# Kernel tuning notes

Measured on AMD Instinct MI355X. Metric: run time of the kernel, lower is better.

The kernel has to match this reference:

```python
import jax, jax.numpy as jnp
from jax import lax
import numpy as np

B, T, N = 64, 512, 80
HT, HV, HI = 512, 1024, 512  # textual, visual, ilstm hidden sizes


def setup_inputs() -> dict:
    key = jax.random.key(0)
    ks = jax.random.split(key, 12)
    s = 0.02
    return {
        "h_v": jax.random.normal(ks[0], (B, T, HV), jnp.float32),
        "h_s": jax.random.normal(ks[1], (B, N, HT), jnp.float32),
        "W_S": jax.random.normal(ks[2], (HI, HT), jnp.float32) * s,
        "b_S": jnp.zeros((HI,), jnp.float32),
        "W_V": jax.random.normal(ks[3], (HI, HV), jnp.float32) * s,
        "b_V": jnp.zeros((HI,), jnp.float32),
        "W_R": jax.random.normal(ks[4], (HI, HI), jnp.float32) * s,
        "b_R": jnp.zeros((HI,), jnp.float32),
        "W_w": jax.random.normal(ks[5], (1, HI), jnp.float32) * s,
        "b_w": jnp.zeros((1,), jnp.float32),
        "W_ih": jax.random.normal(ks[6], (4 * HI, HT + HV), jnp.float32) * s,
        "b_ih": jnp.zeros((4 * HI,), jnp.float32),
        "W_hh": jax.random.normal(ks[7], (4 * HI, HI), jnp.float32) * s,
        "b_hh": jnp.zeros((4 * HI,), jnp.float32),
    }


def reference(h_v, h_s, W_S, b_S, W_V, b_V, W_R, b_R, W_w, b_w, W_ih, b_ih, W_hh, b_hh):
    n_batch, T_, _ = h_v.shape
    Hi = W_R.shape[0]
    dt = h_v.dtype
    # loop-invariant textual projection, hoisted: (B, N, Hi)
    S_proj = jnp.einsum('bnt,it->bni', h_s, W_S) + b_S
    # visual projection for all timesteps: (B, T, Hi)
    V_proj = jnp.einsum('btv,iv->bti', h_v, W_V) + b_V

    def step(carry, xs):
        h_prev, c_prev = carry
        v_t, hv_t = xs  # (B, Hi), (B, Hv)
        r_proj = h_prev @ W_R.T + b_R  # (B, Hi)
        pre = jnp.tanh(S_proj + (r_proj + v_t)[:, None, :])  # (B, N, Hi)
        beta = jnp.einsum('bni,i->bn', pre, W_w[0]) + b_w[0]  # (B, N)
        # NOTE: faithful to source -- softmax over the BATCH dim (dim=0)
        alpha = jax.nn.softmax(beta, axis=0)
        H_t_s = jnp.einsum('bnt,bn->bt', h_s, alpha)  # (B, Ht)
        r_t = jnp.concatenate([hv_t, H_t_s], axis=1)  # (B, Hv+Ht)
        gates = r_t @ W_ih.T + b_ih + h_prev @ W_hh.T + b_hh  # (B, 4Hi)
        i_g, f_g, g_g, o_g = jnp.split(gates, 4, axis=1)
        c_new = jax.nn.sigmoid(f_g) * c_prev + jax.nn.sigmoid(i_g) * jnp.tanh(g_g)
        h_new = jax.nn.sigmoid(o_g) * jnp.tanh(c_new)
        return (h_new, c_new), h_new

    init = (jnp.zeros((n_batch, Hi), dt), jnp.zeros((n_batch, Hi), dt))
    xs = (jnp.swapaxes(V_proj, 0, 1), jnp.swapaxes(h_v, 0, 1))  # time-major
    _, hs = lax.scan(step, init, xs)  # (T, B, Hi)
    return jnp.swapaxes(hs, 0, 1)  # (B, T, Hi)
```

## Files before the change

kernel.cpp:

```cpp
#include <hip/hip_runtime.h>


typedef unsigned short ushort_t;
typedef unsigned int uint_t;
typedef __attribute__((ext_vector_type(8))) short bf16x8;
typedef __attribute__((ext_vector_type(4))) float f32x4;

#define MFMA_BF16 __builtin_amdgcn_mfma_f32_16x16x32_bf16

__device__ __forceinline__ float bf2f(ushort_t u) {
  return __builtin_bit_cast(float, (uint_t)u << 16);
}
__device__ __forceinline__ ushort_t f2bf(float f) {
  uint_t u = __builtin_bit_cast(uint_t, f);
  u += 0x7FFFu + ((u >> 16) & 1u);
  return (ushort_t)(u >> 16);
}
__device__ __forceinline__ uint_t pk(float lo, float hi) {
  return (uint_t)f2bf(lo) | ((uint_t)f2bf(hi) << 16);
}
__device__ __forceinline__ void stage16(ushort_t* dst, const float* src) {
  float4 a = *(const float4*)src,     b = *(const float4*)(src + 4);
  float4 c = *(const float4*)(src + 8), d = *(const float4*)(src + 12);
  uint4 lo = { pk(a.x,a.y), pk(a.z,a.w), pk(b.x,b.y), pk(b.z,b.w) };
  uint4 hi = { pk(c.x,c.y), pk(c.z,c.w), pk(d.x,d.y), pk(d.z,d.w) };
  *(uint4*)dst = lo; *(uint4*)(dst + 8) = hi;
}
__device__ __forceinline__ bf16x8 cvt8(const float* src) {
  float4 a = *(const float4*)src, b = *(const float4*)(src + 4);
  uint4 u = { pk(a.x,a.y), pk(a.z,a.w), pk(b.x,b.y), pk(b.z,b.w) };
  return __builtin_bit_cast(bf16x8, u);
}
__device__ __forceinline__ float tanh_(float x) {
  float e = __expf(2.f * x);
  return 1.f - 2.f * __builtin_amdgcn_rcpf(e + 1.f);
}
__device__ __forceinline__ float sigm_(float x) {
  return __builtin_amdgcn_rcpf(1.f + __expf(-x));
}

__device__ __forceinline__ float ldcg_f(const float* p) {
  return __hip_atomic_load(p, __ATOMIC_RELAXED, __HIP_MEMORY_SCOPE_AGENT);
}
__device__ __forceinline__ void stcg_f(float* p, float v) {
  __hip_atomic_store(p, v, __ATOMIC_RELAXED, __HIP_MEMORY_SCOPE_AGENT);
}
__device__ __forceinline__ uint_t ldcg_u(const uint_t* p) {
  return __hip_atomic_load(p, __ATOMIC_RELAXED, __HIP_MEMORY_SCOPE_AGENT);
}
__device__ __forceinline__ void stcg_u(uint_t* p, uint_t v) {
  __hip_atomic_store(p, v, __ATOMIC_RELAXED, __HIP_MEMORY_SCOPE_AGENT);
}

__global__ __launch_bounds__(256) void cvt_kernel(
    const float* __restrict__ in, ushort_t* __restrict__ out, int n4) {
  int i = blockIdx.x * blockDim.x + threadIdx.x;
  if (i < n4) {
    float4 v = ((const float4*)in)[i];
    uint2 r = { pk(v.x, v.y), pk(v.z, v.w) };
    ((uint2*)out)[i] = r;
  }
}

__global__ __launch_bounds__(256) void pack_frag_kernel(
    const float* __restrict__ src, int ld, int coff,
    ushort_t* __restrict__ out, int mode, int lkc) {
  size_t o = ((size_t)blockIdx.x * 256 + threadIdx.x) * 8;
  int lane = (int)((o >> 3) & 63);
  int kc   = (int)((o >> 9) & ((1u << lkc) - 1u));
  int tile = (int)(o >> (9 + lkc));
  int row  = mode ? ((tile & 3) * 512 + (tile >> 2) * 16 + (lane & 15))
                  : (tile * 16 + (lane & 15));
  int col  = kc * 32 + (lane >> 4) * 8;
  const float* s = &src[(size_t)row * ld + coff + col];
  float4 a = *(const float4*)s, b = *(const float4*)(s + 4);
  uint4 u = { pk(a.x,a.y), pk(a.z,a.w), pk(b.x,b.y), pk(b.z,b.w) };
  *(uint4*)&out[o] = u;
}

__global__ __launch_bounds__(256) void gemm_bt(
    const float* __restrict__ A, int lda,
    const float* __restrict__ W, int ldw,
    const float* __restrict__ bias1,
    ushort_t* __restrict__ out, int ldo, int K, int tmaj)
{
  __shared__ __align__(16) ushort_t sA[128][32];
  __shared__ __align__(16) ushort_t sW[128][32];
  const int tid = threadIdx.x;
  const int col0 = blockIdx.x * 128, row0 = blockIdx.y * 128;
  const int lane = tid & 63, wv = tid >> 6;
  const int wr = (wv & 1) * 64, wc = (wv >> 1) * 64;
  const int fr = lane & 15, quad = lane >> 4;
  const int sr = tid >> 1, skk = (tid & 1) * 16;
  f32x4 acc[4][4] = {};
  for (int k0 = 0; k0 < K; k0 += 32) {
    stage16(&sA[sr][skk], &A[(size_t)(row0 + sr) * lda + k0 + skk]);
    stage16(&sW[sr][skk], &W[(size_t)(col0 + sr) * ldw + k0 + skk]);
    __syncthreads();
    bf16x8 af[4], wf[4];
    #pragma unroll
    for (int mt = 0; mt < 4; ++mt) af[mt] = *(const bf16x8*)&sA[wr + mt*16 + fr][quad*8];
    #pragma unroll
    for (int nt = 0; nt < 4; ++nt) wf[nt] = *(const bf16x8*)&sW[wc + nt*16 + fr][quad*8];
    #pragma unroll
    for (int mt = 0; mt < 4; ++mt)
      #pragma unroll
      for (int nt = 0; nt < 4; ++nt)
        acc[mt][nt] = MFMA_BF16(af[mt], wf[nt], acc[mt][nt], 0, 0, 0);
    __syncthreads();
  }
  #pragma unroll
  for (int nt = 0; nt < 4; ++nt) {
    int col = col0 + wc + nt*16 + fr;
    float bs = bias1 ? bias1[col] : 0.f;
    #pragma unroll
    for (int mt = 0; mt < 4; ++mt)
      #pragma unroll
      for (int r = 0; r < 4; ++r) {
        int row = row0 + wr + mt*16 + quad*4 + r;
        int orow = tmaj ? ((row & 511) * 64 + (row >> 9)) : row;
        out[(size_t)orow * ldo + col] = f2bf(acc[mt][nt][r] + bs);
      }
  }
}

__device__ __forceinline__ void spin_gen(unsigned* gen, unsigned g, unsigned* dead) {
  int n = 0;
  while (__hip_atomic_load(gen, __ATOMIC_RELAXED, __HIP_MEMORY_SCOPE_AGENT) == g) {
    __builtin_amdgcn_s_sleep(4);
    if (++n > 20000) {
      __hip_atomic_store(dead, 1u, __ATOMIC_RELAXED, __HIP_MEMORY_SCOPE_AGENT);
      break;
    }
    if ((n & 1023) == 0 &&
        __hip_atomic_load(dead, __ATOMIC_RELAXED, __HIP_MEMORY_SCOPE_AGENT) != 0u)
      break;
  }
}

__device__ __forceinline__ void sync_bar(unsigned* base, unsigned sub,
                                         unsigned sub_last, unsigned* dead) {
  __syncthreads();
  if (threadIdx.x == 0) {
    unsigned* gen = base + 288;
    if (__hip_atomic_load(dead, __ATOMIC_RELAXED, __HIP_MEMORY_SCOPE_AGENT) == 0u) {
      unsigned g = __hip_atomic_load(gen, __ATOMIC_RELAXED, __HIP_MEMORY_SCOPE_AGENT);
      unsigned old = __hip_atomic_fetch_add(base + sub * 32, 1u,
                        __ATOMIC_RELAXED, __HIP_MEMORY_SCOPE_AGENT);
      if (old == sub_last) {
        unsigned r = __hip_atomic_fetch_add(base + 256, 1u,
                        __ATOMIC_RELAXED, __HIP_MEMORY_SCOPE_AGENT);
        if (r == 7u) {
          #pragma unroll
          for (int i = 0; i < 8; ++i)
            __hip_atomic_store(base + i * 32, 0u, __ATOMIC_RELAXED, __HIP_MEMORY_SCOPE_AGENT);
          __hip_atomic_store(base + 256, 0u, __ATOMIC_RELAXED, __HIP_MEMORY_SCOPE_AGENT);
          __builtin_amdgcn_s_waitcnt(0);
          __hip_atomic_store(gen, g + 1u, __ATOMIC_RELAXED, __HIP_MEMORY_SCOPE_AGENT);
        } else {
          spin_gen(gen, g, dead);
        }
      } else {
        spin_gen(gen, g, dead);
      }
    }
  }
  __syncthreads();
}

struct LoopArgs {
  const ushort_t *Sproj, *Vproj, *Xproj;
  const ushort_t *WRf, *Whhf, *Wqf, *Wihf;
  const ushort_t *hsb;
  const float *bR, *Ww, *bih, *bhh, *hv;
  float *ru, *expb, *s4;
  uint_t *hrep, *hsrep;
  unsigned *bar;
  float *out;
};


__global__ __launch_bounds__(512, 2) void loop_kernel(LoopArgs p) {
  const int blk = blockIdx.x, tid = threadIdx.x;
  const int lane = tid & 63, wv = tid >> 6;
  const int fr = lane & 15, quad = lane >> 4;
  const int G = blk >> 6, w6 = blk & 63;
  const int b4 = G * 16 + (w6 & 15), q = w6 >> 4;
  const bool isGate = (w6 < 32);
  const bool isRu   = (w6 >= 32) && (w6 < 36);
  const int jt = w6 & 31;
  const int g = wv & 3, kh = wv >> 2;
  const int ct = ((w6 - 32) & 3) * 8 + wv;

  unsigned* dead = p.bar + 320;
  unsigned* rcnt = p.bar + 384 + G;
  unsigned* gbar = p.bar + 512 + G * 512;

  __shared__ __align__(16) uint_t sH[4096];
  __shared__ __align__(16) float s_ru[512];
  __shared__ __align__(16) float s_ww[512];
  __shared__ __align__(16) float s_red[512];
  __shared__ __align__(16) float s_acc[8][256];
  __shared__ float s_hsv[128];
  __shared__ float s_alpha[80];
  __shared__ float s_hh[256];
  __shared__ float s_bias[64];

  s_ww[tid] = p.Ww[tid];
  if (isGate && tid < 64) {
    int n = (tid >> 4) * 512 + jt * 16 + (tid & 15);
    s_bias[tid] = p.bih[n] + p.bhh[n];
  }
  float c_reg = 0.f;

  bf16x8 wf2[16];
  bf16x8 wfx[16];
  if (isGate) {
    #pragma unroll
    for (int kc = 0; kc < 8; ++kc) {
      int kcg = kh * 8 + kc;
      wf2[kc]     = *(const bf16x8*)&p.Whhf[((size_t)(jt*4+g)*16 + kcg)*512 + lane*8];
      wf2[8 + kc] = *(const bf16x8*)&p.Wqf [((size_t)(jt*4+g)*16 + kcg)*512 + lane*8];
    }
    if (!p.Xproj) {
      #pragma unroll
      for (int kc = 0; kc < 16; ++kc)
        wfx[kc] = *(const bf16x8*)&p.Wihf[((size_t)(jt*4+g)*32 + kh*16 + kc)*512 + lane*8];
    }
  } else if (isRu) {
    #pragma unroll
    for (int kc = 0; kc < 16; ++kc)
      wf2[kc] = *(const bf16x8*)&p.WRf[((size_t)ct*16 + kc)*512 + lane*8];
  }
  __syncthreads();

  f32x4 accA = {};
  for (int t = 0; t < 512; ++t) {
    float x0 = 0.f, x1 = 0.f, x2 = 0.f, x3 = 0.f;
    if (isGate) {
      f32x4 acc = {};
      if (!p.Xproj) {
        int row = G * 16 + fr;
        #pragma unroll
        for (int kc = 0; kc < 16; ++kc) {
          bf16x8 af = cvt8(&p.hv[((size_t)row * 512 + t) * 1024 + kh*512 + kc*32 + quad*8]);
          acc = MFMA_BF16(af, wfx[kc], acc, 0, 0, 0);
        }
      }
      if (t) {
        const uint_t* src = p.hrep + G * 4096;
        uint_t hst[8];
        #pragma unroll
        for (int i = 0; i < 8; ++i) hst[i] = ldcg_u(src + i * 512 + tid);
        #pragma unroll
        for (int i = 0; i < 8; ++i) sH[i * 512 + tid] = hst[i];
        __syncthreads();
        #pragma unroll
        for (int kc = 0; kc < 8; ++kc) {
          int kcg = kh * 8 + kc;
          bf16x8 af = *(const bf16x8*)&sH[kcg * 256 + quad * 64 + fr * 4];
          acc = MFMA_BF16(af, wf2[kc], acc, 0, 0, 0);
        }
      }
      accA = acc;
      if (p.Xproj && tid < 256) {
        const ushort_t* xp = &p.Xproj[(size_t)t * 131072 +
                                      (size_t)(G * 16 + (tid >> 4)) * 2048 + jt * 16 + (tid & 15)];
        x0 = bf2f(xp[0]);    x1 = bf2f(xp[512]);
        x2 = bf2f(xp[1024]); x3 = bf2f(xp[1536]);
      }
    } else if (isRu) {
      f32x4 acc = {};
      if (t) {
        const uint_t* src = p.hrep + G * 4096;
        uint_t hst[8];
        #pragma unroll
        for (int i = 0; i < 8; ++i) hst[i] = ldcg_u(src + i * 512 + tid);
        #pragma unroll
        for (int i = 0; i < 8; ++i) sH[i * 512 + tid] = hst[i];
        __syncthreads();
        #pragma unroll
        for (int kc = 0; kc < 16; ++kc) {
          bf16x8 af = *(const bf16x8*)&sH[kc * 256 + quad * 64 + fr * 4];
          acc = MFMA_BF16(af, wf2[kc], acc, 0, 0, 0);
        }
      }
      #pragma unroll
      for (int r = 0; r < 4; ++r) {
        int row = G * 16 + quad * 4 + r, col = ct * 16 + fr;
        float v = acc[r] + p.bR[col] + bf2f(p.Vproj[(size_t)t * 32768 + row * 512 + col]);
        stcg_f(&p.ru[row * 512 + col], v);
      }
      __syncthreads();
      if (tid == 0)
        __hip_atomic_fetch_add(rcnt, 1u, __ATOMIC_RELAXED, __HIP_MEMORY_SCOPE_AGENT);
    }

    if (tid == 0) {
      unsigned thr = 4u * (unsigned)(t + 1);
      int n = 0;
      while (ldcg_u(rcnt) < thr) {
        __builtin_amdgcn_s_sleep(4);
        if (++n > 20000) {
          stcg_u(dead, 1u);
          break;
        }
        if ((n & 1023) == 0 && ldcg_u(dead) != 0u) break;
      }
    }
    __syncthreads();
    s_ru[tid] = ldcg_f(&p.ru[b4 * 512 + tid]);
    __syncthreads();
    #pragma unroll
    for (int rr = 0; rr < 3; ++rr) {
      int nl = wv + 8 * rr;
      if (nl < 20) {
        int n = q * 20 + nl;
        uint4 sv = *(const uint4*)&p.Sproj[((size_t)(b4 * 80 + n)) * 512 + lane * 8];
        float4 r0 = *(const float4*)&s_ru[lane * 8];
        float4 r1 = *(const float4*)&s_ru[lane * 8 + 4];
        float4 w0 = *(const float4*)&s_ww[lane * 8];
        float4 w1 = *(const float4*)&s_ww[lane * 8 + 4];
        float a = 0.f;
        a += tanh_(bf2f((ushort_t)(sv.x & 0xFFFF)) + r0.x) * w0.x;
        a += tanh_(bf2f((ushort_t)(sv.x >> 16))    + r0.y) * w0.y;
        a += tanh_(bf2f((ushort_t)(sv.y & 0xFFFF)) + r0.z) * w0.z;
        a += tanh_(bf2f((ushort_t)(sv.y >> 16))    + r0.w) * w0.w;
        a += tanh_(bf2f((ushort_t)(sv.z & 0xFFFF)) + r1.x) * w1.x;
        a += tanh_(bf2f((ushort_t)(sv.z >> 16))    + r1.y) * w1.y;
        a += tanh_(bf2f((ushort_t)(sv.w & 0xFFFF)) + r1.z) * w1.z;
        a += tanh_(bf2f((ushort_t)(sv.w >> 16))    + r1.w) * w1.w;
        #pragma unroll
        for (int off = 32; off > 0; off >>= 1) a += __shfl_xor(a, off, 64);
        if (lane == 0) {
          float e = __expf(a);
          stcg_f(&p.expb[(t & 1) * 5120 + n * 64 + b4], e);
          __hip_atomic_fetch_add(&p.s4[(t % 3) * 320 + G * 80 + n], e,
                                 __ATOMIC_RELAXED, __HIP_MEMORY_SCOPE_AGENT);
        }
      }
    }
    sync_bar(p.bar, (unsigned)(blk & 7), 31u, dead);

    if (tid < 80) {
      const float* sc = p.s4 + (t % 3) * 320;
      float s = ldcg_f(sc + tid) + ldcg_f(sc + 80 + tid) +
                ldcg_f(sc + 160 + tid) + ldcg_f(sc + 240 + tid);
      float num = ldcg_f(&p.expb[(t & 1) * 5120 + tid * 64 + b4]);
      s_alpha[tid] = num * __builtin_amdgcn_rcpf(s);
    }
    if (blk == 0 && tid < 320)
      stcg_f(&p.s4[((t + 2) % 3) * 320 + tid], 0.f);
    __syncthreads();
    {
      int nq = tid >> 7, jl = tid & 127;
      const ushort_t* hp = p.hsb + (size_t)b4 * 40960 + q * 128 + jl;
      float part = 0.f;
      #pragma unroll 5
      for (int n0 = 0; n0 < 20; ++n0) {
        int n = nq * 20 + n0;
        part += s_alpha[n] * bf2f(hp[(size_t)n * 512]);
      }
      s_red[tid] = part;
    }
    __syncthreads();
    if (tid < 128)
      s_hsv[tid] = s_red[tid] + s_red[128 + tid] + s_red[256 + tid] + s_red[384 + tid];
    __syncthreads();
    if (tid < 64) {
      int c = q * 128 + tid * 2;
      int kc = c >> 5, qd = (c >> 3) & 3, e2 = (c & 7) >> 1;
      int dw = ((G * 16 + kc) * 4 + qd) * 64 + (b4 & 15) * 4 + e2;
      stcg_u(&p.hsrep[dw], pk(s_hsv[tid * 2], s_hsv[tid * 2 + 1]));
    }
    sync_bar(gbar, (unsigned)(w6 & 7), 7u, dead);

    if (isGate) {
      const uint_t* src = p.hsrep + G * 4096;
      uint_t hst[8];
      #pragma unroll
      for (int i = 0; i < 8; ++i) hst[i] = ldcg_u(src + i * 512 + tid);
      #pragma unroll
      for (int i = 0; i < 8; ++i) sH[i * 512 + tid] = hst[i];
      __syncthreads();
      f32x4 acc = accA;
      #pragma unroll
      for (int kc = 0; kc < 8; ++kc) {
        int kcg = kh * 8 + kc;
        bf16x8 af = *(const bf16x8*)&sH[kcg * 256 + quad * 64 + fr * 4];
        acc = MFMA_BF16(af, wf2[8 + kc], acc, 0, 0, 0);
      }
      #pragma unroll
      for (int r = 0; r < 4; ++r) s_acc[wv][(quad * 4 + r) * 16 + fr] = acc[r];
      __syncthreads();
      if (tid < 256) {
        int b = tid >> 4, jj = tid & 15, bi = tid;
        float g0 = s_acc[0][bi] + s_acc[4][bi] + s_bias[jj];
        float g1 = s_acc[1][bi] + s_acc[5][bi] + s_bias[16 + jj];
        float g2 = s_acc[2][bi] + s_acc[6][bi] + s_bias[32 + jj];
        float g3 = s_acc[3][bi] + s_acc[7][bi] + s_bias[48 + jj];
        if (p.Xproj) { g0 += x0; g1 += x1; g2 += x2; g3 += x3; }
        float ig = sigm_(g0), fg = sigm_(g1), gv = tanh_(g2), og = sigm_(g3);
        float cn = fg * c_reg + ig * gv;
        c_reg = cn;
        float hn = og * tanh_(cn);
        s_hh[bi] = hn;
        p.out[((size_t)(G * 16 + b) * 512 + t) * 512 + jt * 16 + jj] = hn;
      }
      __syncthreads();
      if (tid < 128) {
        int b = tid >> 3, jp = tid & 7;
        int c = jt * 16 + jp * 2;
        int kc = c >> 5, qd = (c >> 3) & 3, e2 = (c & 7) >> 1;
        int dw = ((G * 16 + kc) * 4 + qd) * 64 + b * 4 + e2;
        stcg_u(&p.hrep[dw], pk(s_hh[b * 16 + jp * 2], s_hh[b * 16 + jp * 2 + 1]));
      }
    }
    sync_bar(gbar, (unsigned)(w6 & 7), 7u, dead);
  }
}

extern "C" void kernel_launch(void* const* d_in, const int* in_sizes, int n_in,
                              void* d_out, int out_size, void* d_ws, size_t ws_size,
                              hipStream_t stream) {
  (void)in_sizes; (void)n_in; (void)out_size;
  const float* hv   = (const float*)d_in[0];
  const float* hs   = (const float*)d_in[1];
  const float* W_S  = (const float*)d_in[2];
  const float* b_S  = (const float*)d_in[3];
  const float* W_V  = (const float*)d_in[4];
  const float* b_V  = (const float*)d_in[5];
  const float* W_R  = (const float*)d_in[6];
  const float* b_R  = (const float*)d_in[7];
  const float* W_w  = (const float*)d_in[8];
  const float* W_ih = (const float*)d_in[10];
  const float* b_ih = (const float*)d_in[11];
  const float* W_hh = (const float*)d_in[12];
  const float* b_hh = (const float*)d_in[13];

  char* ws = (char*)d_ws;
  unsigned long long off = 0;
  auto alloc = [&](unsigned long long bytes) {
    unsigned long long pp = off; off += (bytes + 255ull) & ~255ull; return pp;
  };
  ushort_t* Sproj = (ushort_t*)(ws + alloc(5120ull * 512 * 2));
  ushort_t* Vproj = (ushort_t*)(ws + alloc(512ull * 64 * 512 * 2));
  ushort_t* hsb   = (ushort_t*)(ws + alloc(64ull * 80 * 512 * 2));
  ushort_t* WRf   = (ushort_t*)(ws + alloc(512ull * 512 * 2));
  ushort_t* Whhf  = (ushort_t*)(ws + alloc(2048ull * 512 * 2));
  ushort_t* Wqf   = (ushort_t*)(ws + alloc(2048ull * 512 * 2));
  float*    ru    = (float*)(ws + alloc(64ull * 512 * 4));
  float*    expb  = (float*)(ws + alloc(2ull * 64 * 80 * 4));
  unsigned long long zoff = off;
  uint_t*   hrep  = (uint_t*)(ws + alloc(16384ull * 4));
  uint_t*   hsrep = (uint_t*)(ws + alloc(16384ull * 4));
  float*    s4    = (float*)(ws + alloc(3ull * 320 * 4));
  unsigned* bar   = (unsigned*)(ws + alloc(16384));
  unsigned long long zsize = off - zoff;
  unsigned long long tail = off;
  bool precX = ws_size >= tail + 512ull * 64 * 2048 * 2 + 4096;
  ushort_t* Xproj = precX ? (ushort_t*)(ws + tail) : nullptr;
  ushort_t* Wihf  = precX ? nullptr : (ushort_t*)(ws + tail);

  cvt_kernel<<<2560, 256, 0, stream>>>(hs, hsb, 64 * 80 * 512 / 4);
  pack_frag_kernel<<<128, 256, 0, stream>>>(W_R,  512,  0,    WRf,  0, 4);
  pack_frag_kernel<<<512, 256, 0, stream>>>(W_hh, 512,  0,    Whhf, 1, 4);
  pack_frag_kernel<<<512, 256, 0, stream>>>(W_ih, 1536, 1024, Wqf,  1, 4);
  if (!precX)
    pack_frag_kernel<<<1024, 256, 0, stream>>>(W_ih, 1536, 0, Wihf, 1, 5);

  gemm_bt<<<dim3(4, 40), 256, 0, stream>>>(hs, 512, W_S, 512, b_S, Sproj, 512, 512, 0);
  gemm_bt<<<dim3(4, 256), 256, 0, stream>>>(hv, 1024, W_V, 1024, b_V, Vproj, 512, 1024, 1);
  if (precX)
    gemm_bt<<<dim3(16, 256), 256, 0, stream>>>(hv, 1024, W_ih, 1536, nullptr, Xproj, 2048, 1024, 1);

  hipMemsetAsync(ws + zoff, 0, (size_t)zsize, stream);

  LoopArgs la;
  la.Sproj = Sproj; la.Vproj = Vproj; la.Xproj = Xproj;
  la.WRf = WRf; la.Whhf = Whhf; la.Wqf = Wqf; la.Wihf = Wihf;
  la.hsb = hsb;
  la.bR = b_R; la.Ww = W_w; la.bih = b_ih; la.bhh = b_hh; la.hv = hv;
  la.ru = ru; la.expb = expb; la.s4 = s4;
  la.hrep = hrep; la.hsrep = hsrep; la.bar = bar; la.out = (float*)d_out;
  loop_kernel<<<256, 512, 0, stream>>>(la);
}
```

Measured before the change: 11.14 ms.

## Replace generation barriers with monotonic counters and distribute r-projection across gate blocks

```diff
diff --git a/kernel.cpp b/kernel.cpp
--- a/kernel.cpp
+++ b/kernel.cpp
@@ -124,48 +124,16 @@
   }
 }
 
-__device__ __forceinline__ void spin_gen(unsigned* gen, unsigned g, unsigned* dead) {
+__device__ __forceinline__ void spin_ge(unsigned* c, unsigned thr, unsigned* dead) {
   int n = 0;
-  while (__hip_atomic_load(gen, __ATOMIC_RELAXED, __HIP_MEMORY_SCOPE_AGENT) == g) {
-    __builtin_amdgcn_s_sleep(4);
-    if (++n > 20000) {
-      __hip_atomic_store(dead, 1u, __ATOMIC_RELAXED, __HIP_MEMORY_SCOPE_AGENT);
+  while ((int)(__hip_atomic_load(c, __ATOMIC_RELAXED, __HIP_MEMORY_SCOPE_AGENT) - thr) < 0) {
+    __builtin_amdgcn_s_sleep(2);
+    if (++n > 30000) {
+      stcg_u(dead, 1u);
       break;
     }
-    if ((n & 1023) == 0 &&
-        __hip_atomic_load(dead, __ATOMIC_RELAXED, __HIP_MEMORY_SCOPE_AGENT) != 0u)
-      break;
-  }
-}
-
-__device__ __forceinline__ void sync_bar(unsigned* base, unsigned sub,
-                                         unsigned sub_last, unsigned* dead) {
-  __syncthreads();
-  if (threadIdx.x == 0) {
-    unsigned* gen = base + 288;
-    if (__hip_atomic_load(dead, __ATOMIC_RELAXED, __HIP_MEMORY_SCOPE_AGENT) == 0u) {
-      unsigned g = __hip_atomic_load(gen, __ATOMIC_RELAXED, __HIP_MEMORY_SCOPE_AGENT);
-      unsigned old = __hip_atomic_fetch_add(base + sub * 32, 1u,
-                        __ATOMIC_RELAXED, __HIP_MEMORY_SCOPE_AGENT);
-      if (old == sub_last) {
-        unsigned r = __hip_atomic_fetch_add(base + 256, 1u,
-                        __ATOMIC_RELAXED, __HIP_MEMORY_SCOPE_AGENT);
-        if (r == 7u) {
-          #pragma unroll
-          for (int i = 0; i < 8; ++i)
-            __hip_atomic_store(base + i * 32, 0u, __ATOMIC_RELAXED, __HIP_MEMORY_SCOPE_AGENT);
-          __hip_atomic_store(base + 256, 0u, __ATOMIC_RELAXED, __HIP_MEMORY_SCOPE_AGENT);
-          __builtin_amdgcn_s_waitcnt(0);
-          __hip_atomic_store(gen, g + 1u, __ATOMIC_RELAXED, __HIP_MEMORY_SCOPE_AGENT);
-        } else {
-          spin_gen(gen, g, dead);
-        }
-      } else {
-        spin_gen(gen, g, dead);
-      }
-    }
-  }
-  __syncthreads();
+    if ((n & 15) == 0 && ldcg_u(dead) != 0u) break;
+  }
 }
 
 struct LoopArgs {
@@ -187,20 +155,22 @@
   const int G = blk >> 6, w6 = blk & 63;
   const int b4 = G * 16 + (w6 & 15), q = w6 >> 4;
   const bool isGate = (w6 < 32);
-  const bool isRu   = (w6 >= 32) && (w6 < 36);
   const int jt = w6 & 31;
   const int g = wv & 3, kh = wv >> 2;
-  const int ct = ((w6 - 32) & 3) * 8 + wv;
-
-  unsigned* dead = p.bar + 320;
-  unsigned* rcnt = p.bar + 384 + G;
-  unsigned* gbar = p.bar + 512 + G * 512;
+
+  unsigned* dead  = p.bar + 3584;
+  unsigned* rcnt  = p.bar + G * 32;
+  unsigned* hscnt = p.bar + 128 + G * 32;
+  unsigned* hwcnt = p.bar + 256 + G * 32;
+  unsigned* cnt0  = p.bar + 512;
 
   __shared__ __align__(16) uint_t sH[4096];
   __shared__ __align__(16) float s_ru[512];
   __shared__ __align__(16) float s_ww[512];
   __shared__ __align__(16) float s_red[512];
   __shared__ __align__(16) float s_acc[8][256];
+  __shared__ __align__(16) ushort_t sSp[20][512];
+  __shared__ __align__(16) ushort_t sHsb[80][128];
   __shared__ float s_hsv[128];
   __shared__ float s_alpha[80];
   __shared__ float s_hh[256];
@@ -211,9 +181,22 @@
     int n = (tid >> 4) * 512 + jt * 16 + (tid & 15);
     s_bias[tid] = p.bih[n] + p.bhh[n];
   }
+  float brv = 0.f;
+  if (isGate && tid < 256) brv = p.bR[jt * 16 + (tid & 15)];
+  for (int i = tid; i < 1280; i += 512) {
+    int nl = i >> 6, c8 = (i & 63) * 8;
+    *(uint4*)&sSp[nl][c8] =
+        *(const uint4*)&p.Sproj[((size_t)(b4 * 80 + q * 20 + nl)) * 512 + c8];
+  }
+  for (int i = tid; i < 1280; i += 512) {
+    int n = i >> 4, c8 = (i & 15) * 8;
+    *(uint4*)&sHsb[n][c8] =
+        *(const uint4*)&p.hsb[(size_t)b4 * 40960 + (size_t)n * 512 + q * 128 + c8];
+  }
   float c_reg = 0.f;
 
   bf16x8 wf2[16];
+  bf16x8 wfR[2];
   bf16x8 wfx[16];
   if (isGate) {
     #pragma unroll
@@ -222,22 +205,31 @@
       wf2[kc]     = *(const bf16x8*)&p.Whhf[((size_t)(jt*4+g)*16 + kcg)*512 + lane*8];
       wf2[8 + kc] = *(const bf16x8*)&p.Wqf [((size_t)(jt*4+g)*16 + kcg)*512 + lane*8];
     }
+    #pragma unroll
+    for (int i = 0; i < 2; ++i)
+      wfR[i] = *(const bf16x8*)&p.WRf[((size_t)jt*16 + wv*2 + i)*512 + lane*8];
     if (!p.Xproj) {
       #pragma unroll
       for (int kc = 0; kc < 16; ++kc)
         wfx[kc] = *(const bf16x8*)&p.Wihf[((size_t)(jt*4+g)*32 + kh*16 + kc)*512 + lane*8];
     }
-  } else if (isRu) {
-    #pragma unroll
-    for (int kc = 0; kc < 16; ++kc)
-      wf2[kc] = *(const bf16x8*)&p.WRf[((size_t)ct*16 + kc)*512 + lane*8];
   }
   __syncthreads();
 
   f32x4 accA = {};
   for (int t = 0; t < 512; ++t) {
-    float x0 = 0.f, x1 = 0.f, x2 = 0.f, x3 = 0.f;
+    float x0 = 0.f, x1 = 0.f, x2 = 0.f, x3 = 0.f, vv = 0.f;
     if (isGate) {
+      if (tid < 256) {
+        if (p.Xproj) {
+          const ushort_t* xp = &p.Xproj[(size_t)t * 131072 +
+                                        (size_t)(G * 16 + (tid >> 4)) * 2048 + jt * 16 + (tid & 15)];
+          x0 = bf2f(xp[0]);    x1 = bf2f(xp[512]);
+          x2 = bf2f(xp[1024]); x3 = bf2f(xp[1536]);
+        }
+        vv = bf2f(p.Vproj[(size_t)t * 32768 +
+                          (size_t)(G * 16 + (tid >> 4)) * 512 + jt * 16 + (tid & 15)]);
+      }
       f32x4 acc = {};
       if (!p.Xproj) {
         int row = G * 16 + fr;
@@ -247,7 +239,10 @@
           acc = MFMA_BF16(af, wfx[kc], acc, 0, 0, 0);
         }
       }
+      f32x4 accR = {};
       if (t) {
+        if (tid == 0) spin_ge(hwcnt, 32u * (unsigned)t, dead);
+        __syncthreads();
         const uint_t* src = p.hrep + G * 4096;
         uint_t hst[8];
         #pragma unroll
@@ -255,6 +250,25 @@
         #pragma unroll
         for (int i = 0; i < 8; ++i) sH[i * 512 + tid] = hst[i];
         __syncthreads();
+        #pragma unroll
+        for (int i = 0; i < 2; ++i) {
+          bf16x8 af = *(const bf16x8*)&sH[(wv*2 + i) * 256 + quad * 64 + fr * 4];
+          accR = MFMA_BF16(af, wfR[i], accR, 0, 0, 0);
+        }
+      }
+      #pragma unroll
+      for (int r = 0; r < 4; ++r) s_acc[wv][(quad * 4 + r) * 16 + fr] = accR[r];
+      __syncthreads();
+      if (tid < 256) {
+        float s = s_acc[0][tid] + s_acc[1][tid] + s_acc[2][tid] + s_acc[3][tid] +
+                  s_acc[4][tid] + s_acc[5][tid] + s_acc[6][tid] + s_acc[7][tid] +
+                  brv + vv;
+        stcg_f(&p.ru[(size_t)(G * 16 + (tid >> 4)) * 512 + jt * 16 + (tid & 15)], s);
+      }
+      __syncthreads();
+      if (tid == 0)
+        __hip_atomic_fetch_add(rcnt, 1u, __ATOMIC_RELAXED, __HIP_MEMORY_SCOPE_AGENT);
+      if (t) {
         #pragma unroll
         for (int kc = 0; kc < 8; ++kc) {
           int kcg = kh * 8 + kc;
@@ -263,51 +277,9 @@
         }
       }
       accA = acc;
-      if (p.Xproj && tid < 256) {
-        const ushort_t* xp = &p.Xproj[(size_t)t * 131072 +
-                                      (size_t)(G * 16 + (tid >> 4)) * 2048 + jt * 16 + (tid & 15)];
-        x0 = bf2f(xp[0]);    x1 = bf2f(xp[512]);
-        x2 = bf2f(xp[1024]); x3 = bf2f(xp[1536]);
-      }
-    } else if (isRu) {
-      f32x4 acc = {};
-      if (t) {
-        const uint_t* src = p.hrep + G * 4096;
-        uint_t hst[8];
-        #pragma unroll
-        for (int i = 0; i < 8; ++i) hst[i] = ldcg_u(src + i * 512 + tid);
-        #pragma unroll
-        for (int i = 0; i < 8; ++i) sH[i * 512 + tid] = hst[i];
-        __syncthreads();
-        #pragma unroll
-        for (int kc = 0; kc < 16; ++kc) {
-          bf16x8 af = *(const bf16x8*)&sH[kc * 256 + quad * 64 + fr * 4];
-          acc = MFMA_BF16(af, wf2[kc], acc, 0, 0, 0);
-        }
-      }
-      #pragma unroll
-      for (int r = 0; r < 4; ++r) {
-        int row = G * 16 + quad * 4 + r, col = ct * 16 + fr;
-        float v = acc[r] + p.bR[col] + bf2f(p.Vproj[(size_t)t * 32768 + row * 512 + col]);
-        stcg_f(&p.ru[row * 512 + col], v);
-      }
-      __syncthreads();
-      if (tid == 0)
-        __hip_atomic_fetch_add(rcnt, 1u, __ATOMIC_RELAXED, __HIP_MEMORY_SCOPE_AGENT);
-    }
-
-    if (tid == 0) {
-      unsigned thr = 4u * (unsigned)(t + 1);
-      int n = 0;
-      while (ldcg_u(rcnt) < thr) {
-        __builtin_amdgcn_s_sleep(4);
-        if (++n > 20000) {
-          stcg_u(dead, 1u);
-          break;
-        }
-        if ((n & 1023) == 0 && ldcg_u(dead) != 0u) break;
-      }
-    }
+    }
+
+    if (tid == 0) spin_ge(rcnt, 32u * (unsigned)(t + 1), dead);
     __syncthreads();
     s_ru[tid] = ldcg_f(&p.ru[b4 * 512 + tid]);
     __syncthreads();
@@ -316,7 +288,7 @@
       int nl = wv + 8 * rr;
       if (nl < 20) {
         int n = q * 20 + nl;
-        uint4 sv = *(const uint4*)&p.Sproj[((size_t)(b4 * 80 + n)) * 512 + lane * 8];
+        uint4 sv = *(const uint4*)&sSp[nl][lane * 8];
         float4 r0 = *(const float4*)&s_ru[lane * 8];
         float4 r1 = *(const float4*)&s_ru[lane * 8 + 4];
         float4 w0 = *(const float4*)&s_ww[lane * 8];
@@ -340,26 +312,29 @@
         }
       }
     }
-    sync_bar(p.bar, (unsigned)(blk & 7), 31u, dead);
+    __syncthreads();
+    if (tid < 20)
+      __hip_atomic_fetch_add(cnt0 + (q * 20 + tid) * 32, 1u,
+                             __ATOMIC_RELAXED, __HIP_MEMORY_SCOPE_AGENT);
 
     if (tid < 80) {
+      spin_ge(cnt0 + tid * 32, 64u * (unsigned)(t + 1), dead);
       const float* sc = p.s4 + (t % 3) * 320;
       float s = ldcg_f(sc + tid) + ldcg_f(sc + 80 + tid) +
                 ldcg_f(sc + 160 + tid) + ldcg_f(sc + 240 + tid);
       float num = ldcg_f(&p.expb[(t & 1) * 5120 + tid * 64 + b4]);
       s_alpha[tid] = num * __builtin_amdgcn_rcpf(s);
     }
+    __syncthreads();
     if (blk == 0 && tid < 320)
       stcg_f(&p.s4[((t + 2) % 3) * 320 + tid], 0.f);
-    __syncthreads();
     {
       int nq = tid >> 7, jl = tid & 127;
-      const ushort_t* hp = p.hsb + (size_t)b4 * 40960 + q * 128 + jl;
       float part = 0.f;
       #pragma unroll 5
       for (int n0 = 0; n0 < 20; ++n0) {
         int n = nq * 20 + n0;
-        part += s_alpha[n] * bf2f(hp[(size_t)n * 512]);
+        part += s_alpha[n] * bf2f(sHsb[n][jl]);
       }
       s_red[tid] = part;
     }
@@ -373,9 +348,13 @@
       int dw = ((G * 16 + kc) * 4 + qd) * 64 + (b4 & 15) * 4 + e2;
       stcg_u(&p.hsrep[dw], pk(s_hsv[tid * 2], s_hsv[tid * 2 + 1]));
     }
-    sync_bar(gbar, (unsigned)(w6 & 7), 7u, dead);
+    __syncthreads();
+    if (tid == 0)
+      __hip_atomic_fetch_add(hscnt, 1u, __ATOMIC_RELAXED, __HIP_MEMORY_SCOPE_AGENT);
 
     if (isGate) {
+      if (tid == 0) spin_ge(hscnt, 64u * (unsigned)(t + 1), dead);
+      __syncthreads();
       const uint_t* src = p.hsrep + G * 4096;
       uint_t hst[8];
       #pragma unroll
@@ -399,7 +378,7 @@
         float g1 = s_acc[1][bi] + s_acc[5][bi] + s_bias[16 + jj];
         float g2 = s_acc[2][bi] + s_acc[6][bi] + s_bias[32 + jj];
         float g3 = s_acc[3][bi] + s_acc[7][bi] + s_bias[48 + jj];
-        if (p.Xproj) { g0 += x0; g1 += x1; g2 += x2; g3 += x3; }
+        g0 += x0; g1 += x1; g2 += x2; g3 += x3;
         float ig = sigm_(g0), fg = sigm_(g1), gv = tanh_(g2), og = sigm_(g3);
         float cn = fg * c_reg + ig * gv;
         c_reg = cn;
@@ -415,8 +394,10 @@
         int dw = ((G * 16 + kc) * 4 + qd) * 64 + b * 4 + e2;
         stcg_u(&p.hrep[dw], pk(s_hh[b * 16 + jp * 2], s_hh[b * 16 + jp * 2 + 1]));
       }
-    }
-    sync_bar(gbar, (unsigned)(w6 & 7), 7u, dead);
+      __syncthreads();
+      if (tid == 0)
+        __hip_atomic_fetch_add(hwcnt, 1u, __ATOMIC_RELAXED, __HIP_MEMORY_SCOPE_AGENT);
+    }
   }
 }
 
```

After: 10.17 ms. 8.7% less time.
